# Kernel tuning notes

Hardware: AMD Instinct MI355X
Metric: run time of the kernel (lower is better)

The kernel has to match this reference:

```python
import jax, jax.numpy as jnp
import numpy as np

EPS = 1e-5
WSZ = 8
DH = 32


def _ln_chan(x, g, b):
    # channel LayerNorm over dim=1 of (B,C,H,W), biased variance
    mu = jnp.mean(x, axis=1, keepdims=True)
    var = jnp.mean((x - mu) ** 2, axis=1, keepdims=True)
    return (x - mu) / jnp.sqrt(var + EPS) * g[None, :, None, None] + b[None, :, None, None]


def _conv_transpose2d(x, w, b, stride, pad):
    # torch ConvTranspose2d: w is (C_in, C_out, kh, kw)
    k = w.shape[2]
    wf = jnp.flip(w, (2, 3)).transpose(1, 0, 2, 3)  # (O, I, kh, kw)
    out = jax.lax.conv_general_dilated(
        x, wf, window_strides=(1, 1),
        padding=[(k - 1 - pad, k - 1 - pad)] * 2,
        lhs_dilation=(stride, stride),
        dimension_numbers=("NCHW", "OIHW", "NCHW"))
    return out + b[None, :, None, None]


def _rope_cs(wh, ww, dh, dtype):
    quarter = dh // 4
    freq = 1.0 / (10000.0 ** (jnp.arange(quarter, dtype=dtype) / quarter))
    th = jnp.arange(wh, dtype=dtype)[:, None] * freq          # (wh, q)
    tw = jnp.arange(ww, dtype=dtype)[:, None] * freq          # (ww, q)
    th = jnp.broadcast_to(th[:, None, :], (wh, ww, quarter)).reshape(wh * ww, quarter)
    tw = jnp.broadcast_to(tw[None, :, :], (wh, ww, quarter)).reshape(wh * ww, quarter)
    theta = jnp.concatenate([th, tw], axis=-1)                # (L, dh/2)
    cos = jnp.concatenate([jnp.cos(theta), jnp.cos(theta)], axis=-1)  # (L, dh)
    sin = jnp.concatenate([jnp.sin(theta), jnp.sin(theta)], axis=-1)
    return cos, sin


def _rot_half(x):
    x1, x2 = jnp.split(x, 2, axis=-1)
    return jnp.concatenate([-x2, x1], axis=-1)


def _attn_block(x, g, b, wqkv, wout, bout, shifted):
    B, C, H, W = x.shape
    heads = C // DH
    xn = _ln_chan(x, g, b)
    if shifted:
        xn = jnp.roll(xn, shift=(-(WSZ // 2), -(WSZ // 2)), axis=(2, 3))
    nh, nw = H // WSZ, W // WSZ
    # window partition: (B,C,H,W) -> (B*nh*nw, L, C), L = WSZ*WSZ
    t = xn.reshape(B, C, nh, WSZ, nw, WSZ).transpose(0, 2, 4, 3, 5, 1)
    t = t.reshape(B * nh * nw, WSZ * WSZ, C)
    qkv = t @ wqkv.T                                           # (Bw, L, 3C)
    q, k, v = jnp.split(qkv, 3, axis=-1)

    def split_heads(a):
        return a.reshape(a.shape[0], a.shape[1], heads, DH).transpose(0, 2, 1, 3)
    q, k, v = map(split_heads, (q, k, v))                      # (Bw, h, L, d)
    cos, sin = _rope_cs(WSZ, WSZ, DH, q.dtype)                 # (L, d)
    q = q * cos + _rot_half(q) * sin
    k = k * cos + _rot_half(k) * sin
    scale = DH ** -0.5
    att = jax.nn.softmax(jnp.einsum("bhid,bhjd->bhij", q * scale, k), axis=-1)
    out = jnp.einsum("bhij,bhjd->bhid", att, v)                # (Bw, h, L, d)
    out = out.transpose(0, 2, 1, 3).reshape(B * nh * nw, WSZ * WSZ, C)
    out = out @ wout.T + bout
    out = out.reshape(B, nh, nw, WSZ, WSZ, C).transpose(0, 5, 1, 3, 2, 4).reshape(B, C, H, W)
    if shifted:
        out = jnp.roll(out, shift=(WSZ // 2, WSZ // 2), axis=(2, 3))
    return out


def _ff(x, g, b, w1, b1, w2, b2):
    xn = _ln_chan(x, g, b)
    h = jnp.einsum("bchw,oc->bohw", xn, w1) + b1[None, :, None, None]
    h = jax.nn.gelu(h)
    return jnp.einsum("bchw,oc->bohw", h, w2) + b2[None, :, None, None]


def _forward(x, ct_w2, ct_b2, ct_w4, ct_b4,
             a1_g, a1_b, a1_wqkv, a1_wout, a1_bout,
             f1_g, f1_b, f1_w1, f1_b1, f1_w2, f1_b2,
             a2_g, a2_b, a2_wqkv, a2_wout, a2_bout,
             f2_g, f2_b, f2_w1, f2_b1, f2_w2, f2_b2):
    # CrossExpandLayer: kernels [2,4], stride 2, padding (k-2)//2
    y2 = _conv_transpose2d(x, ct_w2, ct_b2, stride=2, pad=0)
    y4 = _conv_transpose2d(x, ct_w4, ct_b4, stride=2, pad=1)
    h = jnp.concatenate([y2, y4], axis=1)                      # (B, dim_out, 2H, 2W)
    h = h + _attn_block(h, a1_g, a1_b, a1_wqkv, a1_wout, a1_bout, shifted=False)
    h = h + _ff(h, f1_g, f1_b, f1_w1, f1_b1, f1_w2, f1_b2)
    h = h + _attn_block(h, a2_g, a2_b, a2_wqkv, a2_wout, a2_bout, shifted=True)
    h = h + _ff(h, f2_g, f2_b, f2_w1, f2_b1, f2_w2, f2_b2)
    return h


def setup_inputs() -> dict:
    key = jax.random.key(0)
    ks = jax.random.split(key, 32)
    DIM_IN, DIM = 512, 256
    MULT = 4
    s = 0.02
    inp = {"x": jax.random.normal(ks[0], (2, DIM_IN, 64, 128), dtype=jnp.float32)}
    # CrossExpandLayer: dim_scales = [128, 128]
    inp["ct_w2"] = jax.random.normal(ks[1], (DIM_IN, DIM // 2, 2, 2), jnp.float32) * s
    inp["ct_b2"] = jnp.zeros((DIM // 2,), jnp.float32)
    inp["ct_w4"] = jax.random.normal(ks[2], (DIM_IN, DIM // 2, 4, 4), jnp.float32) * s
    inp["ct_b4"] = jnp.zeros((DIM // 2,), jnp.float32)
    for i, pre in enumerate(["a1", "a2"]):
        inp[pre + "_g"] = jnp.ones((DIM,), jnp.float32)
        inp[pre + "_b"] = jnp.zeros((DIM,), jnp.float32)
        inp[pre + "_wqkv"] = jax.random.normal(ks[3 + 2 * i], (3 * DIM, DIM), jnp.float32) * s
        inp[pre + "_wout"] = jax.random.normal(ks[4 + 2 * i], (DIM, DIM), jnp.float32) * s
        inp[pre + "_bout"] = jnp.zeros((DIM,), jnp.float32)
    for i, pre in enumerate(["f1", "f2"]):
        inp[pre + "_g"] = jnp.ones((DIM,), jnp.float32)
        inp[pre + "_b"] = jnp.zeros((DIM,), jnp.float32)
        inp[pre + "_w1"] = jax.random.normal(ks[10 + 2 * i], (MULT * DIM, DIM), jnp.float32) * s
        inp[pre + "_b1"] = jnp.zeros((MULT * DIM,), jnp.float32)
        inp[pre + "_w2"] = jax.random.normal(ks[11 + 2 * i], (DIM, MULT * DIM), jnp.float32) * s
        inp[pre + "_b2"] = jnp.zeros((DIM,), jnp.float32)
    return inp


def reference(x, ct_w2, ct_b2, ct_w4, ct_b4,
              a1_g, a1_b, a1_wqkv, a1_wout, a1_bout,
              f1_g, f1_b, f1_w1, f1_b1, f1_w2, f1_b2,
              a2_g, a2_b, a2_wqkv, a2_wout, a2_bout,
              f2_g, f2_b, f2_w1, f2_b1, f2_w2, f2_b2):
    return _forward(x, ct_w2, ct_b2, ct_w4, ct_b4,
                    a1_g, a1_b, a1_wqkv, a1_wout, a1_bout,
                    f1_g, f1_b, f1_w1, f1_b1, f1_w2, f1_b2,
                    a2_g, a2_b, a2_wqkv, a2_wout, a2_bout,
                    f2_g, f2_b, f2_w1, f2_b1, f2_w2, f2_b2)
```

## Files before the change

### kernel.cpp

```cpp
#include <hip/hip_runtime.h>
#include <hip/hip_bf16.h>
#include <math.h>

typedef __bf16 bf16_t;
typedef __bf16 bf16x8 __attribute__((ext_vector_type(8)));
typedef float  f32x4 __attribute__((ext_vector_type(4)));

constexpr int B_  = 2;
constexpr int CIN = 512, HI = 64, WI = 128;
constexpr int C_  = 256, H_ = 128, W_ = 256;
constexpr int NTOK = B_ * H_ * W_;
constexpr int NWIN = 1024;

__device__ __forceinline__ unsigned short f2bu(float x) {
    return __builtin_bit_cast(unsigned short, (bf16_t)x);
}

__global__ __launch_bounds__(256) void k_rope(float* __restrict__ rope) {
    int i = blockIdx.x * 256 + threadIdx.x;
    if (i >= 2048) return;
    int l = i >> 5, d = i & 31;
    int j = d & 15;
    int ly = l >> 3, lx = l & 7;
    float fr = powf(10000.f, -(float)(j & 7) / 8.f);
    float t = (j < 8 ? (float)ly : (float)lx) * fr;
    rope[i]        = cosf(t);
    rope[2048 + i] = sinf(t);
}

struct CvtSeg { const float* s; bf16_t* d; unsigned n; };
struct CvtParams { CvtSeg seg[8]; };

__global__ __launch_bounds__(256) void k_cvt(CvtParams P) {
    unsigned base = (blockIdx.x * 256u + threadIdx.x) * 4u;
    for (int s = 0; s < 8; s++) {
        unsigned n = P.seg[s].n;
        if (base < n) {
            float4 v = *(const float4*)(P.seg[s].s + base);
            ushort4 o;
            o.x = f2bu(v.x); o.y = f2bu(v.y); o.z = f2bu(v.z); o.w = f2bu(v.w);
            *(ushort4*)(P.seg[s].d + base) = o;
            return;
        }
        base -= n;
    }
}

__global__ __launch_bounds__(256) void k_trx(const float* __restrict__ x,
                                             bf16_t* __restrict__ xT) {
    __shared__ float t[64][65];
    int pos0 = blockIdx.x << 6;
    int ci0  = blockIdx.y << 6;
    int b    = blockIdx.z;
    int tid = threadIdx.x;
    int cpos = tid & 63, rb = tid >> 6;
    const float* src = x + ((size_t)(b * CIN + ci0) << 13) + pos0;
    #pragma unroll
    for (int i = 0; i < 16; i++) {
        int ci = rb + (i << 2);
        t[ci][cpos] = src[((size_t)ci << 13) + cpos];
    }
    __syncthreads();
    int row = tid >> 2, q = tid & 3;
    bf16_t* dst = xT + ((size_t)((b << 13) + pos0 + row) << 9) + ci0 + (q << 4);
    union { uint4 u[2]; unsigned short us[16]; } o;
    #pragma unroll
    for (int e = 0; e < 16; e++)
        o.us[e] = f2bu(t[(q << 4) + e][row]);
    *(uint4*)dst = o.u[0];
    *(uint4*)(dst + 8) = o.u[1];
}

__global__ __launch_bounds__(256) void k_bmat(const float* __restrict__ w2,
                                              const float* __restrict__ w4,
                                              const float* __restrict__ cb2,
                                              const float* __restrict__ cb4,
                                              bf16_t* __restrict__ B512,
                                              bf16_t* __restrict__ B2048,
                                              float* __restrict__ cbias) {
    int idx = blockIdx.x * 256 + threadIdx.x;
    if (idx < 262144) {
        int ci = idx & 511, o = (idx >> 9) & 127, p = idx >> 16;
        int rp = p >> 1, rq = p & 1;
        B512[idx] = (bf16_t)w2[((ci * 128 + o) * 2 + rp) * 2 + rq];
        if (idx < 256) cbias[idx] = idx < 128 ? cb2[idx] : cb4[idx - 128];
    } else {
        int i4 = idx - 262144;
        int k = i4 & 2047, o2 = (i4 >> 11) & 127, p = i4 >> 18;
        int ci = k & 511, t = k >> 9;
        int rp = p >> 1, rq = p & 1, a = t >> 1, c = t & 1;
        int kh = 3 - rp - 2 * a, kw = 3 - rq - 2 * c;
        B2048[i4] = (bf16_t)w4[((ci * 128 + o2) * 4 + kh) * 4 + kw];
    }
}

__device__ __forceinline__ int winmap_pos(int idx, int shift) {
    int win = idx >> 6, l = idx & 63;
    int b = win >> 9, wy = (win >> 5) & 15, wx = win & 31;
    int y = ((wy << 3) + (l >> 3) + shift) & 127;
    int x = ((wx << 3) + (l & 7) + shift) & 255;
    return (b << 15) + (y << 8) + x;
}

__device__ __forceinline__ float gelu_tanh(float x) {
    float u = 1.5957691216057308f * (x + 0.044715f * x * x * x);
    return x - x * __builtin_amdgcn_rcpf(__expf(u) + 1.f);
}

__device__ __forceinline__ int swz(int row, int byteoff) {
    return (row << 7) + (byteoff ^ ((row & 7) << 4));
}

template<int MODE>
__device__ __forceinline__ void gemm_body(
    char* smem,
    const bf16_t* __restrict__ A, const bf16_t* __restrict__ Bw,
    const float* __restrict__ bias, bf16_t* __restrict__ Cb,
    float* __restrict__ Hres, const float* __restrict__ rope,
    int K, int ldc, int pshift, int colbase)
{
    char* Asb = smem;
    char* Bsb = smem + 16384;
    const int tid = threadIdx.x;

    int gx = gridDim.x;
    int bx = blockIdx.x, by = blockIdx.y;
    if ((gridDim.y & 7) == 0) {
        int lin = by * gx + bx;
        int grp = gx << 3;
        int q = lin / grp, r = lin - q * grp;
        by = (r & 7) + (q << 3);
        bx = r >> 3;
    }
    const int m0 = by << 7, n0 = bx << 7;

    const int w = tid >> 6, l = tid & 63;
    const int wm = (w >> 1) << 6, wn = (w & 1) << 6;
    const int r16 = l & 15, r4 = l >> 4;
    const int arow = tid >> 3, abyte = (tid & 7) << 4;

    const bf16_t* Ag = A + (size_t)(m0 + arow) * K + ((tid & 7) << 3);
    const bf16_t* Bg = Bw + (size_t)(n0 + arow) * K + ((tid & 7) << 3);

    f32x4 acc[4][4] = {};
    uint4 ra[4], rb[4];
    #pragma unroll
    for (int i = 0; i < 4; i++) {
        ra[i] = *(const uint4*)(Ag + (size_t)(i << 5) * K);
        rb[i] = *(const uint4*)(Bg + (size_t)(i << 5) * K);
    }
    for (int kt = 0; kt < K; kt += 64) {
        __syncthreads();
        #pragma unroll
        for (int i = 0; i < 4; i++) {
            *(uint4*)(Asb + swz(arow + (i << 5), abyte)) = ra[i];
            *(uint4*)(Bsb + swz(arow + (i << 5), abyte)) = rb[i];
        }
        __syncthreads();
        if (kt + 64 < K) {
            #pragma unroll
            for (int i = 0; i < 4; i++) {
                ra[i] = *(const uint4*)(Ag + (size_t)(i << 5) * K + kt + 64);
                rb[i] = *(const uint4*)(Bg + (size_t)(i << 5) * K + kt + 64);
            }
        }
        #pragma unroll
        for (int kk = 0; kk < 2; kk++) {
            bf16x8 af[4], bfr[4];
            #pragma unroll
            for (int f = 0; f < 4; f++)
                af[f] = *(const bf16x8*)(Asb + swz(wm + (f << 4) + r16, (kk << 6) + (r4 << 4)));
            #pragma unroll
            for (int f = 0; f < 4; f++)
                bfr[f] = *(const bf16x8*)(Bsb + swz(wn + (f << 4) + r16, (kk << 6) + (r4 << 4)));
            #pragma unroll
            for (int fm = 0; fm < 4; fm++)
                #pragma unroll
                for (int fn = 0; fn < 4; fn++)
                    acc[fm][fn] = __builtin_amdgcn_mfma_f32_16x16x32_bf16(
                        af[fm], bfr[fn], acc[fm][fn], 0, 0, 0);
        }
    }

    float* Lt = (float*)smem;
    const int wgrp = wn >> 6;
    #pragma unroll
    for (int p2 = 0; p2 < 2; p2++) {
        __syncthreads();
        if (wgrp == p2) {
            #pragma unroll
            for (int fm = 0; fm < 4; fm++) {
                int lrow = wm + (fm << 4) + (r4 << 2);
                #pragma unroll
                for (int fn = 0; fn < 4; fn++) {
                    f32x4 v = acc[fm][fn];
                    int lcol = (fn << 4) + r16;
                    #pragma unroll
                    for (int j = 0; j < 4; j++)
                        Lt[(lrow + j) * 72 + lcol] = v[j];
                }
            }
        }
        __syncthreads();
        if constexpr (MODE == 0) {
            const int c0 = (tid & 7) << 3;
            const int gcol = n0 + (p2 << 6) + c0;
            const int which = gcol >> 8;
            const int dbase = c0 & 31;
            const int pc = c0 ^ 16;
            const float sc = (which == 0) ? 0.17677669529663687f : 1.f;
            #pragma unroll
            for (int rnd = 0; rnd < 4; rnd++) {
                int row = (tid >> 3) + (rnd << 5);
                int lidx = (m0 + row) & 63;
                float vv[8];
                *(float4*)(vv)     = *(const float4*)(Lt + row * 72 + c0);
                *(float4*)(vv + 4) = *(const float4*)(Lt + row * 72 + c0 + 4);
                union { uint4 q; unsigned short us[8]; } o;
                if (which < 2) {
                    float pp[8];
                    *(float4*)(pp)     = *(const float4*)(Lt + row * 72 + pc);
                    *(float4*)(pp + 4) = *(const float4*)(Lt + row * 72 + pc + 4);
                    #pragma unroll
                    for (int i = 0; i < 8; i++) {
                        int d = dbase + i;
                        float cs = rope[lidx * 32 + d];
                        float sn = rope[2048 + lidx * 32 + d];
                        float rot = (d < 16) ? -pp[i] : pp[i];
                        o.us[i] = f2bu((vv[i] * cs + rot * sn) * sc);
                    }
                } else {
                    #pragma unroll
                    for (int i = 0; i < 8; i++) o.us[i] = f2bu(vv[i]);
                }
                *(uint4*)(Cb + (size_t)(m0 + row) * ldc + gcol) = o.q;
            }
        } else {
            const int c0 = (tid & 15) << 2;
            const int gcol = colbase + n0 + (p2 << 6) + c0;
            float bb[4];
            *(float4*)bb = *(const float4*)(bias + gcol);
            const int rp = pshift >> 1, rq = pshift & 1;
            #pragma unroll
            for (int rnd = 0; rnd < 8; rnd++) {
                int row = (tid >> 4) + (rnd << 4);
                float4 v = *(const float4*)(Lt + row * 72 + c0);
                int idx = m0 + row;
                int b = idx >> 13, u = (idx >> 7) & 63, vpos = idx & 127;
                int pos = (b << 15) + (((u << 1) + rp) << 8) + (vpos << 1) + rq;
                float* hp = Hres + ((size_t)pos << 8) + gcol;
                float4 r2;
                r2.x = v.x + bb[0]; r2.y = v.y + bb[1];
                r2.z = v.z + bb[2]; r2.w = v.w + bb[3];
                *(float4*)hp = r2;
            }
        }
    }
}

__global__ __launch_bounds__(256) void k_qkv_gemm(
    const bf16_t* __restrict__ A, const bf16_t* __restrict__ Bw,
    bf16_t* __restrict__ Cb, const float* __restrict__ rope, int K, int ldc) {
    __shared__ char smem[36864];
    gemm_body<0>(smem, A, Bw, nullptr, Cb, nullptr, rope, K, ldc, 0, 0);
}

__global__ __launch_bounds__(256) void k_conv2(
    const bf16_t* __restrict__ xT, const bf16_t* __restrict__ B512,
    const float* __restrict__ cbias, float* __restrict__ h_t) {
    __shared__ char smem[36864];
    int par = blockIdx.z;
    gemm_body<4>(smem, xT, B512 + ((size_t)par << 16), cbias, nullptr,
                 h_t, nullptr, 512, 0, par, 0);
}

__global__ __launch_bounds__(256) void k_conv4(const bf16_t* __restrict__ xT,
                                               const bf16_t* __restrict__ B2048,
                                               const float* __restrict__ cbias,
                                               float* __restrict__ h_t) {
    __shared__ char smem[36864];
    char* Asb = smem;
    char* Bsb = smem + 16384;
    const int tid = threadIdx.x;
    const int par = blockIdx.z;
    const int rp = par >> 1, rq = par & 1;
    const int m0 = blockIdx.y << 7;

    const int w = tid >> 6, l = tid & 63;
    const int wm = (w >> 1) << 6, wn = (w & 1) << 6;
    const int r16 = l & 15, r4 = l >> 4;
    const int arow = tid >> 3, abyte = (tid & 7) << 4;
    const int klane = (tid & 7) << 3;

    int mr_[4], u_[4], v_[4];
    #pragma unroll
    for (int i = 0; i < 4; i++) {
        mr_[i] = m0 + arow + (i << 5);
        u_[i] = (mr_[i] >> 7) & 63;
        v_[i] = mr_[i] & 127;
    }
    const bf16_t* Bp = B2048 + ((size_t)par << 18);

    auto loadA = [&](int c, uint4* r) {
        int t = c >> 3, ci0 = (c & 7) << 6;
        int dh = rp - 1 + (t >> 1), dw = rq - 1 + (t & 1);
        int off = (dh << 7) + dw;
        #pragma unroll
        for (int i = 0; i < 4; i++) {
            bool ok = ((unsigned)(u_[i] + dh) < (unsigned)HI) &&
                      ((unsigned)(v_[i] + dw) < (unsigned)WI);
            if (ok)
                r[i] = *(const uint4*)(xT + ((size_t)(mr_[i] + off) << 9) + ci0 + klane);
            else
                r[i] = uint4{0, 0, 0, 0};
        }
    };
    auto loadB = [&](int c, uint4* r) {
        #pragma unroll
        for (int i = 0; i < 4; i++)
            r[i] = *(const uint4*)(Bp + ((size_t)(arow + (i << 5)) << 11)
                                   + (c << 6) + klane);
    };

    f32x4 acc[4][4] = {};
    uint4 ra[4], rb[4];
    loadA(0, ra);
    loadB(0, rb);
    for (int c = 0; c < 32; c++) {
        __syncthreads();
        #pragma unroll
        for (int i = 0; i < 4; i++) {
            *(uint4*)(Asb + swz(arow + (i << 5), abyte)) = ra[i];
            *(uint4*)(Bsb + swz(arow + (i << 5), abyte)) = rb[i];
        }
        __syncthreads();
        if (c + 1 < 32) {
            loadA(c + 1, ra);
            loadB(c + 1, rb);
        }
        #pragma unroll
        for (int kk = 0; kk < 2; kk++) {
            bf16x8 af[4], bfr[4];
            #pragma unroll
            for (int f = 0; f < 4; f++)
                af[f] = *(const bf16x8*)(Asb + swz(wm + (f << 4) + r16, (kk << 6) + (r4 << 4)));
            #pragma unroll
            for (int f = 0; f < 4; f++)
                bfr[f] = *(const bf16x8*)(Bsb + swz(wn + (f << 4) + r16, (kk << 6) + (r4 << 4)));
            #pragma unroll
            for (int fm = 0; fm < 4; fm++)
                #pragma unroll
                for (int fn = 0; fn < 4; fn++)
                    acc[fm][fn] = __builtin_amdgcn_mfma_f32_16x16x32_bf16(
                        af[fm], bfr[fn], acc[fm][fn], 0, 0, 0);
        }
    }

    float* Lt = (float*)smem;
    const int wgrp = wn >> 6;
    #pragma unroll
    for (int p2 = 0; p2 < 2; p2++) {
        __syncthreads();
        if (wgrp == p2) {
            #pragma unroll
            for (int fm = 0; fm < 4; fm++) {
                int lrow = wm + (fm << 4) + (r4 << 2);
                #pragma unroll
                for (int fn = 0; fn < 4; fn++) {
                    f32x4 v = acc[fm][fn];
                    int lcol = (fn << 4) + r16;
                    #pragma unroll
                    for (int j = 0; j < 4; j++)
                        Lt[(lrow + j) * 72 + lcol] = v[j];
                }
            }
        }
        __syncthreads();
        const int c0 = (tid & 15) << 2;
        const int gcol = 128 + (p2 << 6) + c0;
        float bb[4];
        *(float4*)bb = *(const float4*)(cbias + gcol);
        #pragma unroll
        for (int rnd = 0; rnd < 8; rnd++) {
            int row = (tid >> 4) + (rnd << 4);
            float4 v = *(const float4*)(Lt + row * 72 + c0);
            int idx = m0 + row;
            int b = idx >> 13, u = (idx >> 7) & 63, vpos = idx & 127;
            int pos = (b << 15) + (((u << 1) + rp) << 8) + (vpos << 1) + rq;
            float* hp = h_t + ((size_t)pos << 8) + gcol;
            float4 r2;
            r2.x = v.x + bb[0]; r2.y = v.y + bb[1];
            r2.z = v.z + bb[2]; r2.w = v.w + bb[3];
            *(float4*)hp = r2;
        }
    }
}

__global__ __launch_bounds__(256) void k_attnp(const bf16_t* __restrict__ qkv,
                                               const bf16_t* __restrict__ wout,
                                               const float* __restrict__ bout,
                                               float* __restrict__ h_t,
                                               int win_base, int shift) {
    __shared__ char smem[18944];
    bf16_t* Vs = (bf16_t*)smem;
    const int tid = threadIdx.x;
    const int w = tid >> 6, l = tid & 63;
    const int r16 = l & 15, r4 = l >> 4;
    bf16_t* Ps = (bf16_t*)(smem + 4608) + w * 1152;
    bf16_t* Os = (bf16_t*)(smem + 13824) + w * 640;
    const int winl = blockIdx.x;
    const bf16_t* qb = qkv + ((size_t)winl << 6) * 768;

    f32x4 acc[16] = {};
    for (int h = 0; h < 8; h++) {
        const int ho = h << 5;
        __syncthreads();
        {
            int tok = tid >> 2, dq = (tid & 3) << 3;
            bf16x8 vv = *(const bf16x8*)(qb + tok * 768 + 512 + ho + dq);
            #pragma unroll
            for (int e = 0; e < 8; e++)
                Vs[(dq + e) * 68 + tok] = vv[e];
        }
        __syncthreads();
        bf16x8 qa = *(const bf16x8*)(qb + (w * 16 + r16) * 768 + ho + r4 * 8);
        f32x4 s[4];
        #pragma unroll
        for (int jt = 0; jt < 4; jt++) {
            f32x4 z = {};
            bf16x8 kb = *(const bf16x8*)(qb + (jt * 16 + r16) * 768 + 256 + ho + r4 * 8);
            s[jt] = __builtin_amdgcn_mfma_f32_16x16x32_bf16(qa, kb, z, 0, 0, 0);
        }
        #pragma unroll
        for (int j = 0; j < 4; j++) {
            float m = fmaxf(fmaxf(s[0][j], s[1][j]), fmaxf(s[2][j], s[3][j]));
            #pragma unroll
            for (int o = 8; o > 0; o >>= 1) m = fmaxf(m, __shfl_xor(m, o));
            float sum = 0.f;
            #pragma unroll
            for (int jt = 0; jt < 4; jt++) { s[jt][j] = __expf(s[jt][j] - m); sum += s[jt][j]; }
            #pragma unroll
            for (int o = 8; o > 0; o >>= 1) sum += __shfl_xor(sum, o);
            float inv = 1.f / sum;
            #pragma unroll
            for (int jt = 0; jt < 4; jt++)
                Ps[(r4 * 4 + j) * 72 + jt * 16 + r16] = (bf16_t)(s[jt][j] * inv);
        }
        f32x4 ov[2] = {};
        #pragma unroll
        for (int kt = 0; kt < 2; kt++) {
            bf16x8 pa = *(const bf16x8*)(Ps + r16 * 72 + kt * 32 + r4 * 8);
            #pragma unroll
            for (int nt = 0; nt < 2; nt++) {
                bf16x8 vb = *(const bf16x8*)(Vs + (nt * 16 + r16) * 68 + kt * 32 + r4 * 8);
                ov[nt] = __builtin_amdgcn_mfma_f32_16x16x32_bf16(pa, vb, ov[nt], 0, 0, 0);
            }
        }
        #pragma unroll
        for (int nt = 0; nt < 2; nt++)
            #pragma unroll
            for (int j = 0; j < 4; j++)
                Os[(r4 * 4 + j) * 40 + nt * 16 + r16] = (bf16_t)ov[nt][j];
        bf16x8 oa = *(const bf16x8*)(Os + r16 * 40 + r4 * 8);
        #pragma unroll
        for (int nt = 0; nt < 16; nt++) {
            bf16x8 wb = *(const bf16x8*)(wout + (nt * 16 + r16) * 256 + ho + r4 * 8);
            acc[nt] = __builtin_amdgcn_mfma_f32_16x16x32_bf16(oa, wb, acc[nt], 0, 0, 0);
        }
    }

    float* Lt = (float*)smem;
    const int gwin = win_base + winl;
    #pragma unroll
    for (int p = 0; p < 4; p++) {
        __syncthreads();
        #pragma unroll
        for (int t2 = 0; t2 < 4; t2++) {
            f32x4 v = acc[p * 4 + t2];
            #pragma unroll
            for (int j = 0; j < 4; j++)
                Lt[(w * 16 + r4 * 4 + j) * 68 + t2 * 16 + r16] = v[j];
        }
        __syncthreads();
        int row = tid >> 2, c0 = (tid & 3) << 4;
        int pos = winmap_pos((gwin << 6) + row, shift);
        float* hp = h_t + ((size_t)pos << 8) + (p << 6) + c0;
        const float* bp = bout + (p << 6) + c0;
        #pragma unroll
        for (int i = 0; i < 4; i++) {
            float4 v = *(const float4*)(Lt + row * 68 + c0 + (i << 2));
            float4 bb = *(const float4*)(bp + (i << 2));
            float4 r = *(const float4*)(hp + (i << 2));
            r.x += v.x + bb.x; r.y += v.y + bb.y;
            r.z += v.z + bb.z; r.w += v.w + bb.w;
            *(float4*)(hp + (i << 2)) = r;
        }
    }
}

__global__ __launch_bounds__(512, 4) void k_ffn(const bf16_t* __restrict__ xn,
                                                const bf16_t* __restrict__ w1,
                                                const float* __restrict__ b1,
                                                const bf16_t* __restrict__ w2,
                                                const float* __restrict__ b2,
                                                float* __restrict__ h_t) {
    __shared__ char smem[49152];
    bf16_t* Xs = (bf16_t*)smem;
    bf16_t* Hs = (bf16_t*)(smem + 32768);
    const int tid = threadIdx.x;
    const int w = tid >> 6, l = tid & 63;
    const int r16 = l & 15, r4 = l >> 4;
    const int tok0 = blockIdx.x << 6;

    const bf16_t* xsrc = xn + ((size_t)tok0 << 8);
    #pragma unroll
    for (int i = 0; i < 4; i++) {
        int gi = i * 512 + tid;
        int row = gi >> 5;
        int col = (gi & 31) << 3;
        uint4 v = *(const uint4*)(xsrc + gi * 8);
        *(uint4*)(Xs + (row << 8) + (col ^ ((row & 7) << 3))) = v;
    }
    __syncthreads();

    f32x4 acc2[4][2] = {};
    #pragma unroll
    for (int hc = 0; hc < 8; hc++) {
        f32x4 acc1[4] = {};
        #pragma unroll
        for (int kk = 0; kk < 8; kk++) {
            bf16x8 af[4];
            #pragma unroll
            for (int fm = 0; fm < 4; fm++)
                af[fm] = *(const bf16x8*)(Xs + (((fm << 4) + r16) << 8)
                          + (((kk << 5) + (r4 << 3)) ^ ((r16 & 7) << 3)));
            int nh = (hc << 7) + (w << 4) + r16;
            bf16x8 bf1 = *(const bf16x8*)(w1 + ((size_t)nh << 8) + (kk << 5) + (r4 << 3));
            #pragma unroll
            for (int fm = 0; fm < 4; fm++)
                acc1[fm] = __builtin_amdgcn_mfma_f32_16x16x32_bf16(
                    af[fm], bf1, acc1[fm], 0, 0, 0);
        }
        if (hc) __syncthreads();
        {
            int hcol = (w << 4) + r16;
            float bi = b1[(hc << 7) + hcol];
            #pragma unroll
            for (int fm = 0; fm < 4; fm++) {
                #pragma unroll
                for (int j = 0; j < 4; j++) {
                    int row = (fm << 4) + (r4 << 2) + j;
                    Hs[(row << 7) + (hcol ^ ((row & 7) << 3))] =
                        (bf16_t)gelu_tanh(acc1[fm][j] + bi);
                }
            }
        }
        __syncthreads();
        #pragma unroll
        for (int kk = 0; kk < 4; kk++) {
            bf16x8 a2[4];
            #pragma unroll
            for (int fm = 0; fm < 4; fm++)
                a2[fm] = *(const bf16x8*)(Hs + (((fm << 4) + r16) << 7)
                          + (((kk << 5) + (r4 << 3)) ^ ((r16 & 7) << 3)));
            bf16x8 b2f[2];
            #pragma unroll
            for (int fn = 0; fn < 2; fn++) {
                int nc = (w << 5) + (fn << 4) + r16;
                b2f[fn] = *(const bf16x8*)(w2 + ((size_t)nc << 10) + (hc << 7)
                           + (kk << 5) + (r4 << 3));
            }
            #pragma unroll
            for (int fm = 0; fm < 4; fm++)
                #pragma unroll
                for (int fn = 0; fn < 2; fn++)
                    acc2[fm][fn] = __builtin_amdgcn_mfma_f32_16x16x32_bf16(
                        a2[fm], b2f[fn], acc2[fm][fn], 0, 0, 0);
        }
    }

    float* Lt = (float*)smem;
    #pragma unroll
    for (int p = 0; p < 2; p++) {
        __syncthreads();
        if ((w >> 2) == p) {
            #pragma unroll
            for (int fm = 0; fm < 4; fm++)
                #pragma unroll
                for (int fn = 0; fn < 2; fn++) {
                    f32x4 v = acc2[fm][fn];
                    int col = ((w & 3) << 5) + (fn << 4) + r16;
                    #pragma unroll
                    for (int j = 0; j < 4; j++)
                        Lt[((fm << 4) + (r4 << 2) + j) * 132 + col] = v[j];
                }
        }
        __syncthreads();
        int row = tid >> 3;
        int c0 = (tid & 7) << 4;
        float* hp = h_t + (((size_t)(tok0 + row)) << 8) + (p << 7) + c0;
        const float* bp = b2 + (p << 7) + c0;
        #pragma unroll
        for (int i = 0; i < 4; i++) {
            float4 v = *(const float4*)(Lt + row * 132 + c0 + (i << 2));
            float4 bb = *(const float4*)(bp + (i << 2));
            float4 r = *(const float4*)(hp + (i << 2));
            r.x += v.x + bb.x; r.y += v.y + bb.y;
            r.z += v.z + bb.z; r.w += v.w + bb.w;
            *(float4*)(hp + (i << 2)) = r;
        }
    }
}

__global__ __launch_bounds__(256) void k_ln(const float* __restrict__ h,
                                            const float* __restrict__ g,
                                            const float* __restrict__ bt,
                                            bf16_t* __restrict__ xn,
                                            int windowed, int shift) {
    int tok = (blockIdx.x << 2) + (threadIdx.x >> 6);
    int l = threadIdx.x & 63;
    float4 v = *(const float4*)(h + ((size_t)tok << 8) + (l << 2));
    float s  = v.x + v.y + v.z + v.w;
    float s2 = v.x * v.x + v.y * v.y + v.z * v.z + v.w * v.w;
    #pragma unroll
    for (int o = 32; o > 0; o >>= 1) { s += __shfl_xor(s, o); s2 += __shfl_xor(s2, o); }
    float mu = s * (1.f / 256.f);
    float rs = rsqrtf(s2 * (1.f / 256.f) - mu * mu + 1e-5f);
    int orow = tok;
    if (windowed) {
        int b = tok >> 15, img = tok & 32767;
        int y2 = ((img >> 8) - shift) & 127;
        int x2 = ((img & 255) - shift) & 255;
        orow = (((b << 9) + ((y2 >> 3) << 5) + (x2 >> 3)) << 6) + ((y2 & 7) << 3) + (x2 & 7);
    }
    int c = l << 2;
    float4 gv = *(const float4*)(g + c);
    float4 bv = *(const float4*)(bt + c);
    ushort4 o;
    o.x = f2bu((v.x - mu) * rs * gv.x + bv.x);
    o.y = f2bu((v.y - mu) * rs * gv.y + bv.y);
    o.z = f2bu((v.z - mu) * rs * gv.z + bv.z);
    o.w = f2bu((v.w - mu) * rs * gv.w + bv.w);
    *(ushort4*)(xn + ((size_t)orow << 8) + c) = o;
}

__global__ __launch_bounds__(256) void k_tr(const float* __restrict__ src,
                                            float* __restrict__ dst) {
    __shared__ float t[64][65];
    int tx = blockIdx.x & 3;
    int ty = blockIdx.x >> 2;
    int tid = threadIdx.x;
    int c = (tx << 6) + (tid & 63), r = tid >> 6;
    #pragma unroll
    for (int i = 0; i < 16; i++)
        t[r + i * 4][tid & 63] = src[(size_t)((ty << 6) + r + i * 4) * 256 + c];
    __syncthreads();
    int tok = (ty << 6) + (tid & 63);
    int c2 = tid >> 6;
    #pragma unroll
    for (int i = 0; i < 16; i++)
        dst[(size_t)((tx << 6) + c2 + i * 4) * 32768 + tok] = t[tid & 63][c2 + i * 4];
}

__global__ __launch_bounds__(256) void k_tr2(const float* __restrict__ ht,
                                             float* __restrict__ out) {
    __shared__ float t[128][65];
    int tk0 = blockIdx.x << 7;
    int c0  = blockIdx.y << 6;
    int tid = threadIdx.x;
    #pragma unroll
    for (int rep = 0; rep < 8; rep++) {
        int idx = rep * 256 + tid;
        int row = idx >> 4, c4 = (idx & 15) << 2;
        float4 v = *(const float4*)(ht + ((size_t)(tk0 + row) << 8) + c0 + c4);
        t[row][c4] = v.x; t[row][c4 + 1] = v.y; t[row][c4 + 2] = v.z; t[row][c4 + 3] = v.w;
    }
    __syncthreads();
    int b = tk0 >> 15, img0 = tk0 & 32767;
    #pragma unroll
    for (int rep = 0; rep < 8; rep++) {
        int idx = rep * 256 + tid;
        int jc = idx & 31, c = idx >> 5;
        float4 v;
        v.x = t[(jc << 2) + 0][c];
        v.y = t[(jc << 2) + 1][c];
        v.z = t[(jc << 2) + 2][c];
        v.w = t[(jc << 2) + 3][c];
        *(float4*)(out + (((size_t)(b << 8) + c0 + c) << 15) + img0 + (jc << 2)) = v;
    }
}

extern "C" void kernel_launch(void* const* d_in, const int* in_sizes, int n_in,
                              void* d_out, int out_size, void* d_ws, size_t ws_size,
                              hipStream_t stream) {
    const float* x     = (const float*)d_in[0];
    const float* ct_w2 = (const float*)d_in[1];
    const float* ct_b2 = (const float*)d_in[2];
    const float* ct_w4 = (const float*)d_in[3];
    const float* ct_b4 = (const float*)d_in[4];
    const float* ag[2]  = {(const float*)d_in[5],  (const float*)d_in[10]};
    const float* abt[2] = {(const float*)d_in[6],  (const float*)d_in[11]};
    const float* awq[2] = {(const float*)d_in[7],  (const float*)d_in[12]};
    const float* awo[2] = {(const float*)d_in[8],  (const float*)d_in[13]};
    const float* abo[2] = {(const float*)d_in[9],  (const float*)d_in[14]};
    const float* fg[2]  = {(const float*)d_in[15], (const float*)d_in[21]};
    const float* fbt[2] = {(const float*)d_in[16], (const float*)d_in[22]};
    const float* fw1[2] = {(const float*)d_in[17], (const float*)d_in[23]};
    const float* fb1[2] = {(const float*)d_in[18], (const float*)d_in[24]};
    const float* fw2[2] = {(const float*)d_in[19], (const float*)d_in[25]};
    const float* fb2[2] = {(const float*)d_in[20], (const float*)d_in[26]};

    char* w = (char*)d_ws;
    auto alloc = [&](size_t bytes) {
        char* p = w; w += (bytes + 255) & ~(size_t)255; return p;
    };
    float*  rope  = (float*)alloc(4096 * 4);
    bf16_t* wqkvb[2] = {(bf16_t*)alloc(196608 * 2), (bf16_t*)alloc(196608 * 2)};
    bf16_t* woutb[2] = {(bf16_t*)alloc(65536 * 2),  (bf16_t*)alloc(65536 * 2)};
    bf16_t* fw1b[2]  = {(bf16_t*)alloc(262144 * 2), (bf16_t*)alloc(262144 * 2)};
    bf16_t* fw2b[2]  = {(bf16_t*)alloc(262144 * 2), (bf16_t*)alloc(262144 * 2)};
    bf16_t* B512  = (bf16_t*)alloc((size_t)262144 * 2);
    bf16_t* B2048 = (bf16_t*)alloc((size_t)1048576 * 2);
    float*  cbias = (float*)alloc(256 * 4);
    bf16_t* xT    = (bf16_t*)alloc((size_t)16384 * 512 * 2);
    char*   XN    = alloc(33554432);
    bf16_t* xn = (bf16_t*)XN;

    size_t usedB = (size_t)(w - (char*)d_ws);
    size_t rem = ws_size > usedB ? ws_size - usedB : 0;
    const size_t HT_BYTES = (size_t)NTOK * C_ * 4;
    bool pathA = rem >= HT_BYTES + (size_t)16777216;
    float* h_t = pathA ? (float*)alloc(HT_BYTES) : (float*)d_out;

    usedB = (size_t)(w - (char*)d_ws);
    size_t Sb = ws_size > usedB ? ws_size - usedB : 0;
    if (Sb > (size_t)134217728) Sb = 134217728;
    char* S = w;

    auto p2f = [](size_t v) -> size_t { size_t r = 1; while ((r << 1) <= v) r <<= 1; return r; };
    int CW = (int)(Sb / 98304 >= 1024 ? 1024 : p2f(Sb / 98304));
    if (CW < 16) CW = 16;

    k_rope<<<8, 256, 0, stream>>>(rope);
    CvtParams P;
    P.seg[0] = { awq[0],  wqkvb[0],  196608 };
    P.seg[1] = { awq[1],  wqkvb[1],  196608 };
    P.seg[2] = { awo[0],  woutb[0],  65536 };
    P.seg[3] = { awo[1],  woutb[1],  65536 };
    P.seg[4] = { fw1[0],  fw1b[0],   262144 };
    P.seg[5] = { fw1[1],  fw1b[1],   262144 };
    P.seg[6] = { fw2[0],  fw2b[0],   262144 };
    P.seg[7] = { fw2[1],  fw2b[1],   262144 };
    unsigned total4 = (196608u * 2 + 65536u * 2 + 262144u * 4) / 4;
    k_cvt<<<(total4 + 255) / 256, 256, 0, stream>>>(P);
    k_bmat<<<5120, 256, 0, stream>>>(ct_w2, ct_w4, ct_b2, ct_b4, B512, B2048, cbias);
    k_trx<<<dim3(128, 8, 2), 256, 0, stream>>>(x, xT);

    k_conv2<<<dim3(1, 128, 4), 256, 0, stream>>>(xT, B512, cbias, h_t);
    k_conv4<<<dim3(1, 128, 4), 256, 0, stream>>>(xT, B2048, cbias, h_t);

    for (int blk = 0; blk < 2; blk++) {
        int shift = blk ? 4 : 0;
        k_ln<<<NTOK / 4, 256, 0, stream>>>(h_t, ag[blk], abt[blk], xn, 1, shift);
        for (int w0 = 0; w0 < NWIN; w0 += CW) {
            bf16_t* qkvc = (bf16_t*)S;
            k_qkv_gemm<<<dim3(6, CW / 2), 256, 0, stream>>>(
                xn + (size_t)w0 * 64 * 256, wqkvb[blk], qkvc, rope, 256, 768);
            k_attnp<<<CW, 256, 0, stream>>>(qkvc, woutb[blk], abo[blk], h_t, w0, shift);
        }
        k_ln<<<NTOK / 4, 256, 0, stream>>>(h_t, fg[blk], fbt[blk], xn, 0, 0);
        k_ffn<<<NTOK / 64, 512, 0, stream>>>(xn, fw1b[blk], fb1[blk],
                                             fw2b[blk], fb2[blk], h_t);
    }

    if (pathA) {
        k_tr2<<<dim3(512, 4), 256, 0, stream>>>(h_t, (float*)d_out);
    } else {
        for (int b = 0; b < 2; b++) {
            hipMemcpyAsync(XN, h_t + (size_t)b * 32768 * 256, 33554432,
                           hipMemcpyDeviceToDevice, stream);
            k_tr<<<2048, 256, 0, stream>>>((const float*)XN,
                                           (float*)d_out + (size_t)b * 256 * 32768);
        }
    }
}
```

Baseline: 1.001 ms.

## Fuse pre-FFN LayerNorm into FFN kernel and widen hidden chunk to 256

The separate LayerNorm launch before the FFN is removed. The FFN kernel now reads fp32 activations, normalizes each token row with a wavefront shuffle reduction, and writes bf16 into shared memory. This saves the round trip of the normalized tensor through global memory. The hidden-dimension chunk grows from 128 to 256, which halves the number of chunk iterations and barriers. In exchange, shared memory rises to 64KB and there are more accumulator registers, which can lower occupancy. Variance is computed as E[x^2]-mu^2, which is less numerically robust. The kernel also reads and writes h_t in place, which looks safe because each block touches only its own rows.

```diff
diff --git a/kernel.cpp b/kernel.cpp
--- a/kernel.cpp
+++ b/kernel.cpp
@@ -498,13 +498,15 @@
     }
 }
 
-__global__ __launch_bounds__(512, 4) void k_ffn(const bf16_t* __restrict__ xn,
+__global__ __launch_bounds__(512, 4) void k_ffn(const float* __restrict__ h_in,
+                                                const float* __restrict__ gam,
+                                                const float* __restrict__ bet,
                                                 const bf16_t* __restrict__ w1,
                                                 const float* __restrict__ b1,
                                                 const bf16_t* __restrict__ w2,
                                                 const float* __restrict__ b2,
                                                 float* __restrict__ h_t) {
-    __shared__ char smem[49152];
+    __shared__ char smem[65536];
     bf16_t* Xs = (bf16_t*)smem;
     bf16_t* Hs = (bf16_t*)(smem + 32768);
     const int tid = threadIdx.x;
@@ -512,21 +514,37 @@
     const int r16 = l & 15, r4 = l >> 4;
     const int tok0 = blockIdx.x << 6;
 
-    const bf16_t* xsrc = xn + ((size_t)tok0 << 8);
-    #pragma unroll
-    for (int i = 0; i < 4; i++) {
-        int gi = i * 512 + tid;
-        int row = gi >> 5;
-        int col = (gi & 31) << 3;
-        uint4 v = *(const uint4*)(xsrc + gi * 8);
-        *(uint4*)(Xs + (row << 8) + (col ^ ((row & 7) << 3))) = v;
+    {
+        const int c = l << 2;
+        float4 gv = *(const float4*)(gam + c);
+        float4 bv = *(const float4*)(bet + c);
+        const float* hsrc = h_in + ((size_t)tok0 << 8);
+        #pragma unroll
+        for (int rep = 0; rep < 8; rep++) {
+            int row = (rep << 3) + w;
+            float4 v = *(const float4*)(hsrc + ((size_t)row << 8) + c);
+            float s  = v.x + v.y + v.z + v.w;
+            float s2 = v.x * v.x + v.y * v.y + v.z * v.z + v.w * v.w;
+            #pragma unroll
+            for (int o = 32; o > 0; o >>= 1) {
+                s += __shfl_xor(s, o); s2 += __shfl_xor(s2, o);
+            }
+            float mu = s * (1.f / 256.f);
+            float rs = rsqrtf(s2 * (1.f / 256.f) - mu * mu + 1e-5f);
+            ushort4 o4;
+            o4.x = f2bu((v.x - mu) * rs * gv.x + bv.x);
+            o4.y = f2bu((v.y - mu) * rs * gv.y + bv.y);
+            o4.z = f2bu((v.z - mu) * rs * gv.z + bv.z);
+            o4.w = f2bu((v.w - mu) * rs * gv.w + bv.w);
+            *(ushort4*)(Xs + (row << 8) + (c ^ ((row & 7) << 3))) = o4;
+        }
     }
     __syncthreads();
 
     f32x4 acc2[4][2] = {};
     #pragma unroll
-    for (int hc = 0; hc < 8; hc++) {
-        f32x4 acc1[4] = {};
+    for (int hc2 = 0; hc2 < 4; hc2++) {
+        f32x4 acc1[2][4] = {};
         #pragma unroll
         for (int kk = 0; kk < 8; kk++) {
             bf16x8 af[4];
@@ -534,40 +552,49 @@
             for (int fm = 0; fm < 4; fm++)
                 af[fm] = *(const bf16x8*)(Xs + (((fm << 4) + r16) << 8)
                           + (((kk << 5) + (r4 << 3)) ^ ((r16 & 7) << 3)));
-            int nh = (hc << 7) + (w << 4) + r16;
-            bf16x8 bf1 = *(const bf16x8*)(w1 + ((size_t)nh << 8) + (kk << 5) + (r4 << 3));
+            bf16x8 b1f[2];
+            #pragma unroll
+            for (int ch = 0; ch < 2; ch++) {
+                int nh = (hc2 << 8) + (ch << 7) + (w << 4) + r16;
+                b1f[ch] = *(const bf16x8*)(w1 + ((size_t)nh << 8) + (kk << 5) + (r4 << 3));
+            }
+            #pragma unroll
+            for (int ch = 0; ch < 2; ch++)
+                #pragma unroll
+                for (int fm = 0; fm < 4; fm++)
+                    acc1[ch][fm] = __builtin_amdgcn_mfma_f32_16x16x32_bf16(
+                        af[fm], b1f[ch], acc1[ch][fm], 0, 0, 0);
+        }
+        if (hc2) __syncthreads();
+        {
+            #pragma unroll
+            for (int ch = 0; ch < 2; ch++) {
+                int hcol = (ch << 7) + (w << 4) + r16;
+                float bi = b1[(hc2 << 8) + hcol];
+                #pragma unroll
+                for (int fm = 0; fm < 4; fm++) {
+                    #pragma unroll
+                    for (int j = 0; j < 4; j++) {
+                        int row = (fm << 4) + (r4 << 2) + j;
+                        Hs[(row << 8) + (hcol ^ ((row & 7) << 3))] =
+                            (bf16_t)gelu_tanh(acc1[ch][fm][j] + bi);
+                    }
+                }
+            }
+        }
+        __syncthreads();
+        #pragma unroll
+        for (int kk = 0; kk < 8; kk++) {
+            bf16x8 a2[4];
             #pragma unroll
             for (int fm = 0; fm < 4; fm++)
-                acc1[fm] = __builtin_amdgcn_mfma_f32_16x16x32_bf16(
-                    af[fm], bf1, acc1[fm], 0, 0, 0);
-        }
-        if (hc) __syncthreads();
-        {
-            int hcol = (w << 4) + r16;
-            float bi = b1[(hc << 7) + hcol];
-            #pragma unroll
-            for (int fm = 0; fm < 4; fm++) {
-                #pragma unroll
-                for (int j = 0; j < 4; j++) {
-                    int row = (fm << 4) + (r4 << 2) + j;
-                    Hs[(row << 7) + (hcol ^ ((row & 7) << 3))] =
-                        (bf16_t)gelu_tanh(acc1[fm][j] + bi);
-                }
-            }
-        }
-        __syncthreads();
-        #pragma unroll
-        for (int kk = 0; kk < 4; kk++) {
-            bf16x8 a2[4];
-            #pragma unroll
-            for (int fm = 0; fm < 4; fm++)
-                a2[fm] = *(const bf16x8*)(Hs + (((fm << 4) + r16) << 7)
+                a2[fm] = *(const bf16x8*)(Hs + (((fm << 4) + r16) << 8)
                           + (((kk << 5) + (r4 << 3)) ^ ((r16 & 7) << 3)));
             bf16x8 b2f[2];
             #pragma unroll
             for (int fn = 0; fn < 2; fn++) {
                 int nc = (w << 5) + (fn << 4) + r16;
-                b2f[fn] = *(const bf16x8*)(w2 + ((size_t)nc << 10) + (hc << 7)
+                b2f[fn] = *(const bf16x8*)(w2 + ((size_t)nc << 10) + (hc2 << 8)
                            + (kk << 5) + (r4 << 3));
             }
             #pragma unroll
@@ -768,8 +795,8 @@
                 xn + (size_t)w0 * 64 * 256, wqkvb[blk], qkvc, rope, 256, 768);
             k_attnp<<<CW, 256, 0, stream>>>(qkvc, woutb[blk], abo[blk], h_t, w0, shift);
         }
-        k_ln<<<NTOK / 4, 256, 0, stream>>>(h_t, fg[blk], fbt[blk], xn, 0, 0);
-        k_ffn<<<NTOK / 64, 512, 0, stream>>>(xn, fw1b[blk], fb1[blk],
+        k_ffn<<<NTOK / 64, 512, 0, stream>>>(h_t, fg[blk], fbt[blk],
+                                             fw1b[blk], fb1[blk],
                                              fw2b[blk], fb2[blk], h_t);
     }
 
```

Result: slower. 1.050 ms (+4.9%).
